# Kernel tuning notes

Measured on AMD Instinct MI355X. Metric: run time of the kernel, lower is better.

## Reference

```python
import jax, jax.numpy as jnp
import numpy as np

B, T_ENC, H2 = 32, 1024, 1024   # H2 = 2*hidden_dim
E = 128                          # embedding_dim == vocab/target size
L = 128                          # decoder timesteps (ground_truth length)
G = 4 * H2                       # LSTM gate dim
IN = E + H2                      # LSTM input dim


def setup_inputs() -> dict:
    key = jax.random.key(0)
    ks = jax.random.split(key, 6)
    s = 0.05
    return {
        "context_tensor": jax.random.normal(ks[0], (B, T_ENC, H2), jnp.float32),
        "ground_truth": jax.random.uniform(ks[1], (B, L, E), jnp.float32),
        "W_ih": jax.random.normal(ks[2], (G, IN), jnp.float32) * s,
        "W_hh": jax.random.normal(ks[3], (G, H2), jnp.float32) * s,
        "b_ih": jnp.zeros((G,), jnp.float32),
        "b_hh": jnp.zeros((G,), jnp.float32),
        "W_out": jax.random.normal(ks[4], (E, 4 * H2 // 2 * 2), jnp.float32)[:, : 2 * H2] * 0,  # placeholder overwritten below
    } | {
        "W_out": jax.random.normal(ks[4], (E, 2 * H2), jnp.float32) * s,
        "b_out": jnp.zeros((E,), jnp.float32),
    }


def reference(context_tensor, ground_truth, W_ih, W_hh, b_ih, b_hh, W_out, b_out):
    Bb, Ll, Ee = ground_truth.shape
    h2 = context_tensor.shape[-1]
    # initial <sos>: one-hot at index 0 (CreateOnehotVariable of zeros)
    onehot0 = jnp.zeros((Bb, Ee), context_tensor.dtype).at[:, 0].set(1.0)
    # input word at step i: onehot0 if i==0 else ground_truth[:, i-1]  (teacher forcing)
    words = jnp.concatenate([onehot0[:, None, :], ground_truth[:, :-1, :]], axis=1)  # [B,L,E]
    ctx0 = context_tensor[:, 0, :]  # [B,2H] -- original always concats frame 0
    xs = jnp.concatenate(
        [words, jnp.broadcast_to(ctx0[:, None, :], (Bb, Ll, h2))], axis=-1
    )  # [B,L,E+2H]
    xs = jnp.swapaxes(xs, 0, 1)  # [L,B,IN]

    def step(carry, x_t):
        h, c = carry
        gates = x_t @ W_ih.T + h @ W_hh.T + (b_ih + b_hh)  # [B,4*2H]
        i_g, f_g, g_g, o_g = jnp.split(gates, 4, axis=-1)
        c = jax.nn.sigmoid(f_g) * c + jax.nn.sigmoid(i_g) * jnp.tanh(g_g)
        h = jax.nn.sigmoid(o_g) * jnp.tanh(c)
        # dot-product attention over listener features
        energy = jnp.einsum("bh,bth->bt", h, context_tensor)
        score = jax.nn.softmax(energy, axis=-1)
        ctx = jnp.einsum("bt,bth->bh", score, context_tensor)
        feat = jnp.concatenate([h, ctx], axis=-1)  # [B,4*hidden]
        pred = jax.nn.log_softmax(feat @ W_out.T + b_out, axis=-1)  # [B,E]
        return (h, c), pred

    h0 = jnp.zeros((Bb, h2), context_tensor.dtype)
    c0 = jnp.zeros((Bb, h2), context_tensor.dtype)
    _, preds = jax.lax.scan(step, (h0, c0), xs)  # [L,B,E]
    return jnp.swapaxes(preds, 0, 1)  # [B,L,E]
```

## Files before the change

kernel.cpp:

```cpp
#include <hip/hip_runtime.h>

#define BATCH 32
#define TENC  1024
#define HD    1024
#define ED    128
#define LL    128
#define GD    4096
#define IND   1152
#define HSTEP (BATCH*HD)

#define HBUF_OFF 131072
#define ARR_OFF  (HBUF_OFF + 129*HSTEP)
#define REL_OFF  (ARR_OFF + 8192)
#define E_OFF    (REL_OFF + 64)
#define P_OFF    (E_OFF + BATCH*LL*TENC)
#define CTX_OFF  (P_OFF + BATCH*LL*TENC)
#define W16_OFF  CTX_OFF

typedef _Float16 h16x2 __attribute__((ext_vector_type(2)));
typedef __fp16   f16x2 __attribute__((ext_vector_type(2)));
typedef _Float16 f16x8v __attribute__((ext_vector_type(8)));
typedef float    f32x4v __attribute__((ext_vector_type(4)));
union CVT { f16x2 f; h16x2 h; unsigned u; };
union U4H8 { uint4 u; f16x8v h; };

__device__ __forceinline__ unsigned pk16(float x, float y) {
  CVT c; c.f = __builtin_amdgcn_cvt_pkrtz(x, y); return c.u;
}
__device__ __forceinline__ float dd2(unsigned a, unsigned b, float c) {
  CVT x{.u = a}, y{.u = b};
  return __builtin_amdgcn_fdot2(x.h, y.h, c, false);
}
__device__ __forceinline__ float sigf(float x) {
  return __builtin_amdgcn_rcpf(1.0f + __expf(-x));
}
__device__ __forceinline__ float tanhf_fast(float x) {
  return 1.0f - 2.0f * __builtin_amdgcn_rcpf(1.0f + __expf(2.0f * x));
}
__device__ __forceinline__ unsigned bfrne(float f) {
  unsigned v = __float_as_uint(f);
  return (v + 0x7fffu + ((v >> 16) & 1u)) >> 16;
}
__device__ __forceinline__ float bf2f(unsigned short u) {
  return __uint_as_float(((unsigned)u) << 16);
}
__device__ __forceinline__ void csth(unsigned short* p, unsigned short v) {
  __hip_atomic_store(p, v, __ATOMIC_RELAXED, __HIP_MEMORY_SCOPE_AGENT);
}
__device__ __forceinline__ void cstu(unsigned* p, unsigned v) {
  __hip_atomic_store(p, v, __ATOMIC_RELAXED, __HIP_MEMORY_SCOPE_AGENT);
}
__device__ __forceinline__ unsigned cldu(const unsigned* p) {
  return __hip_atomic_load(p, __ATOMIC_RELAXED, __HIP_MEMORY_SCOPE_AGENT);
}

__global__ __launch_bounds__(256) void base_kernel(
    const float* __restrict__ ctxt, const float* __restrict__ Wih,
    const float* __restrict__ bih, const float* __restrict__ bhh,
    float* __restrict__ base) {
  int id = blockIdx.x * 256 + threadIdx.x;
  int b = id & (BATCH - 1);
  int g = id >> 5;
  const float4* c4 = reinterpret_cast<const float4*>(ctxt + (size_t)b * TENC * HD);
  const float4* w4 = reinterpret_cast<const float4*>(Wih + (size_t)g * IND + ED);
  float a = 0.f;
#pragma unroll 8
  for (int kk = 0; kk < HD/4; ++kk) {
    float4 c = c4[kk], w = w4[kk];
    a += c.x*w.x + c.y*w.y + c.z*w.z + c.w*w.w;
  }
  base[(size_t)b * GD + g] = a + bih[g] + bhh[g];
}

__global__ __launch_bounds__(256) void packA_kernel(
    const float* __restrict__ Whh, float* __restrict__ ws) {
  uint4* WA = reinterpret_cast<uint4*>(ws + W16_OFF);
  const int t = blockIdx.x * 256 + threadIdx.x;
  const int l = t & 63;
  const int s = (t >> 6) & 1;
  const int w = (t >> 7) & 15;
  const int rg = t >> 11;
  const int m = l & 15;
  const int row = (m & 3) * 1024 + rg * 4 + (m >> 2);
  const int kb = 64 * w + 32 * s + (l >> 4) * 8;
  const float* src = Whh + (size_t)row * 1024 + kb;
  float4 a = *reinterpret_cast<const float4*>(src);
  float4 b = *reinterpret_cast<const float4*>(src + 4);
  uint4 o;
  o.x = pk16(a.x, a.y); o.y = pk16(a.z, a.w);
  o.z = pk16(b.x, b.y); o.w = pk16(b.z, b.w);
  WA[t] = o;
}

__global__ __launch_bounds__(256) void phase0_wordg(
    const float* __restrict__ gt, const float* __restrict__ Wih,
    float* __restrict__ ws) {
  const int mt = blockIdx.x & 31, nt = blockIdx.x >> 5;
  const int r0 = mt * 128, n0 = nt * 128;
  const int tid = threadIdx.x, tx = tid & 15, ty = tid >> 4;
  unsigned short* wg = reinterpret_cast<unsigned short*>(ws + E_OFF);
  __shared__ float At[128][18];
  __shared__ float BtT[16][132];
  float acc[8][8];
#pragma unroll
  for (int i = 0; i < 8; ++i)
#pragma unroll
    for (int j = 0; j < 8; ++j) acc[i][j] = 0.f;

  const int sr = tid >> 1, sc = (tid & 1) * 8;
  for (int kt = 0; kt < 8; ++kt) {
    const int k0 = kt * 16;
    const float* ap = Wih + (size_t)(r0 + sr) * IND + k0 + sc;
    float4 a0 = *reinterpret_cast<const float4*>(ap);
    float4 a1 = *reinterpret_cast<const float4*>(ap + 4);
    const int n = n0 + sr, t = n >> 5, bb = n & 31;
    float4 b0, b1;
    if (t == 0) {
      b0 = make_float4((k0 + sc == 0) ? 1.f : 0.f, 0.f, 0.f, 0.f);
      b1 = make_float4(0.f, 0.f, 0.f, 0.f);
    } else {
      const float* bp = gt + ((size_t)bb * LL + (t - 1)) * ED + k0 + sc;
      b0 = *reinterpret_cast<const float4*>(bp);
      b1 = *reinterpret_cast<const float4*>(bp + 4);
    }
    __syncthreads();
    *reinterpret_cast<float4*>(&At[sr][sc]) = a0;
    *reinterpret_cast<float4*>(&At[sr][sc + 4]) = a1;
    BtT[sc+0][sr] = b0.x; BtT[sc+1][sr] = b0.y; BtT[sc+2][sr] = b0.z; BtT[sc+3][sr] = b0.w;
    BtT[sc+4][sr] = b1.x; BtT[sc+5][sr] = b1.y; BtT[sc+6][sr] = b1.z; BtT[sc+7][sr] = b1.w;
    __syncthreads();
#pragma unroll
    for (int kk2 = 0; kk2 < 8; ++kk2) {
      float2 av[8];
#pragma unroll
      for (int i = 0; i < 8; ++i)
        av[i] = *reinterpret_cast<const float2*>(&At[ty*8 + i][kk2*2]);
      float4 c00 = *reinterpret_cast<const float4*>(&BtT[kk2*2][tx*8]);
      float4 c01 = *reinterpret_cast<const float4*>(&BtT[kk2*2][tx*8 + 4]);
      float4 c10 = *reinterpret_cast<const float4*>(&BtT[kk2*2+1][tx*8]);
      float4 c11 = *reinterpret_cast<const float4*>(&BtT[kk2*2+1][tx*8 + 4]);
#pragma unroll
      for (int i = 0; i < 8; ++i) {
        acc[i][0] += av[i].x*c00.x + av[i].y*c10.x;
        acc[i][1] += av[i].x*c00.y + av[i].y*c10.y;
        acc[i][2] += av[i].x*c00.z + av[i].y*c10.z;
        acc[i][3] += av[i].x*c00.w + av[i].y*c10.w;
        acc[i][4] += av[i].x*c01.x + av[i].y*c11.x;
        acc[i][5] += av[i].x*c01.y + av[i].y*c11.y;
        acc[i][6] += av[i].x*c01.z + av[i].y*c11.z;
        acc[i][7] += av[i].x*c01.w + av[i].y*c11.w;
      }
    }
  }
  const int nb = n0 + tx * 8, t = nb >> 5, b0i = nb & 31;
#pragma unroll
  for (int i = 0; i < 8; ++i) {
    const int row = r0 + ty * 8 + i;
    uint4 pk;
    pk.x = bfrne(acc[i][0]) | (bfrne(acc[i][1]) << 16);
    pk.y = bfrne(acc[i][2]) | (bfrne(acc[i][3]) << 16);
    pk.z = bfrne(acc[i][4]) | (bfrne(acc[i][5]) << 16);
    pk.w = bfrne(acc[i][6]) | (bfrne(acc[i][7]) << 16);
    *reinterpret_cast<uint4*>(wg + ((size_t)t * GD + row) * 32 + b0i) = pk;
  }
}

__global__ __launch_bounds__(1024, 4) void phaseA(float* __restrict__ ws) {
  const int rg = blockIdx.x;
  const int tid = threadIdx.x;
  const int lane = tid & 63;
  const int w = tid >> 6;
  float* base = ws;
  unsigned short* h16 = reinterpret_cast<unsigned short*>(ws + HBUF_OFF);
  unsigned* arr = reinterpret_cast<unsigned*>(ws + ARR_OFF);
  const unsigned short* wg = reinterpret_cast<const unsigned short*>(ws + E_OFF);
  const uint4* WA = reinterpret_cast<const uint4*>(ws + W16_OFF);

  extern __shared__ float smem[];
  uint4* h_lds = reinterpret_cast<uint4*>(smem);
  float* part = smem + 16384;
  float* red  = smem + 24576;

  U4H8 afr0, afr1;
  afr0.u = WA[((size_t)rg * 32 + w * 2 + 0) * 64 + lane];
  afr1.u = WA[((size_t)rg * 32 + w * 2 + 1) * 64 + lane];

  const int rT = tid >> 8, rm = (tid >> 4) & 15, rb = tid & 15;
  const int rbg = rT * 16 + rb;
  const int rrow = (rm & 3) * 1024 + rg * 4 + (rm >> 2);
  float base_r = (tid < 512) ? base[(size_t)rbg * GD + rrow] : 0.f;

  const int cjl = tid >> 5, cb = tid & 31;
  float c_reg = 0.f;

  for (int k = 0; k < LL; ++k) {
    uint4 sv[4];
    const uint4* src = reinterpret_cast<const uint4*>(h16 + (size_t)k * HSTEP);
#pragma unroll
    for (int i = 0; i < 4; ++i) sv[i] = src[tid + 1024 * i];
    float wgv = 0.f;
    if (tid < 512) wgv = bf2f(wg[((size_t)k * GD + rrow) * 32 + rbg]);
#pragma unroll
    for (int i = 0; i < 4; ++i) {
      const int u = tid + 1024 * i;
      h_lds[u ^ ((u >> 7) & 15)] = sv[i];
    }
    __syncthreads();

    f32x4v acc0 = {0.f, 0.f, 0.f, 0.f}, acc1 = acc0;
    {
      const int b0 = lane & 15, b1 = 16 + (lane & 15);
      const int k0u = 8 * w + (lane >> 4);
      U4H8 bf00, bf01, bf10, bf11;
      bf00.u = h_lds[(b0 * 128 + k0u) ^ (b0 & 15)];
      bf10.u = h_lds[(b1 * 128 + k0u) ^ (b1 & 15)];
      bf01.u = h_lds[(b0 * 128 + k0u + 4) ^ (b0 & 15)];
      bf11.u = h_lds[(b1 * 128 + k0u + 4) ^ (b1 & 15)];
      acc0 = __builtin_amdgcn_mfma_f32_16x16x32_f16(afr0.h, bf00.h, acc0, 0, 0, 0);
      acc1 = __builtin_amdgcn_mfma_f32_16x16x32_f16(afr0.h, bf10.h, acc1, 0, 0, 0);
      acc0 = __builtin_amdgcn_mfma_f32_16x16x32_f16(afr1.h, bf01.h, acc0, 0, 0, 0);
      acc1 = __builtin_amdgcn_mfma_f32_16x16x32_f16(afr1.h, bf11.h, acc1, 0, 0, 0);
    }
#pragma unroll
    for (int q = 0; q < 4; ++q) {
      const int m = (lane >> 4) * 4 + q;
      part[(m * 16 + w) * 16 + (lane & 15)] = acc0[q];
      part[((16 + m) * 16 + w) * 16 + (lane & 15)] = acc1[q];
    }
    __syncthreads();

    if (tid < 512) {
      float s = 0.f;
#pragma unroll
      for (int ww = 0; ww < 16; ++ww)
        s += part[((rT * 16 + rm) * 16 + ww) * 16 + rb];
      red[rm * 32 + rbg] = s + wgv + base_r;
    }
    __syncthreads();

    if (tid < 128) {
      float ig = sigf(red[(4 * cjl + 0) * 32 + cb]);
      float fg = sigf(red[(4 * cjl + 1) * 32 + cb]);
      float gg = tanhf_fast(red[(4 * cjl + 2) * 32 + cb]);
      float og = sigf(red[(4 * cjl + 3) * 32 + cb]);
      c_reg = fg * c_reg + ig * gg;
      float hv = og * tanhf_fast(c_reg);
      csth(h16 + (size_t)(k + 1) * HSTEP + (size_t)cb * HD + (rg * 4 + cjl),
           (unsigned short)(pk16(hv, hv) & 0xffffu));
    }

    if (k < LL - 1) {
      __syncthreads();
      const unsigned tgt = (unsigned)(k + 1);
      if (tid == 0) cstu(arr + rg * 32, tgt);
      if (tid < 64) {
        int ok;
        do {
          ok = 1;
#pragma unroll
          for (int q = 0; q < 4; ++q)
            ok &= (cldu(arr + (lane * 4 + q) * 32) >= (unsigned)tgt);
        } while (!__all(ok));
      }
      __syncthreads();
    }
  }
}

__global__ __launch_bounds__(256) void b1_energy(
    const float* __restrict__ ctxt, float* __restrict__ ws) {
  const int b = blockIdx.x >> 4, pt = blockIdx.x & 15;
  const int p0 = pt * 64;
  const int tid = threadIdx.x, tx = tid & 15, ty = tid >> 4;
  const unsigned short* h16 = reinterpret_cast<const unsigned short*>(ws + HBUF_OFF);
  float* E = ws + E_OFF;
  __shared__ unsigned At[128][8];
  __shared__ unsigned CtT[8][64];
  float acc[8][4];
#pragma unroll
  for (int i = 0; i < 8; ++i)
#pragma unroll
    for (int j = 0; j < 4; ++j) acc[i][j] = 0.f;

  const int ar = tid >> 1, ah = tid & 1;
  const int cr = tid >> 2, cq = tid & 3;
  for (int kt = 0; kt < 64; ++kt) {
    const int k0 = kt * 16;
    uint4 u = *reinterpret_cast<const uint4*>(
        h16 + (size_t)(ar + 1) * HSTEP + (size_t)b * HD + k0 + ah * 8);
    const float* cs = ctxt + ((size_t)b * TENC + p0 + cr) * HD + k0 + cq * 4;
    float4 g = *reinterpret_cast<const float4*>(cs);
    __syncthreads();
    *reinterpret_cast<uint4*>(&At[ar][ah * 4]) = u;
    CtT[2*cq][cr]   = pk16(g.x, g.y);
    CtT[2*cq+1][cr] = pk16(g.z, g.w);
    __syncthreads();
#pragma unroll
    for (int kk2 = 0; kk2 < 4; ++kk2) {
      uint2 av[8];
#pragma unroll
      for (int i = 0; i < 8; ++i)
        av[i] = *reinterpret_cast<const uint2*>(&At[ty*8 + i][kk2*2]);
      uint4 cA = *reinterpret_cast<const uint4*>(&CtT[2*kk2][tx*4]);
      uint4 cB = *reinterpret_cast<const uint4*>(&CtT[2*kk2+1][tx*4]);
#pragma unroll
      for (int i = 0; i < 8; ++i) {
        acc[i][0] = dd2(av[i].y, cB.x, dd2(av[i].x, cA.x, acc[i][0]));
        acc[i][1] = dd2(av[i].y, cB.y, dd2(av[i].x, cA.y, acc[i][1]));
        acc[i][2] = dd2(av[i].y, cB.z, dd2(av[i].x, cA.z, acc[i][2]));
        acc[i][3] = dd2(av[i].y, cB.w, dd2(av[i].x, cA.w, acc[i][3]));
      }
    }
  }
#pragma unroll
  for (int i = 0; i < 8; ++i) {
    float* ep = E + ((size_t)b * LL + ty*8 + i) * TENC + p0 + tx*4;
    *reinterpret_cast<float4*>(ep) = make_float4(acc[i][0], acc[i][1], acc[i][2], acc[i][3]);
  }
}

__global__ __launch_bounds__(1024) void b2_softmax(float* __restrict__ ws) {
  const int b = blockIdx.x >> 3, tc = blockIdx.x & 7;
  const int w = threadIdx.x >> 6, lane = threadIdx.x & 63;
  const int t = tc * 16 + w;
  const float* E = ws + E_OFF;
  unsigned* P16 = reinterpret_cast<unsigned*>(ws + P_OFF);
  const float4* e4 = reinterpret_cast<const float4*>(E + ((size_t)b * LL + t) * TENC);
  float4 v[4];
#pragma unroll
  for (int c = 0; c < 4; ++c) v[c] = e4[c * 64 + lane];
  float m = fmaxf(fmaxf(fmaxf(v[0].x, v[0].y), fmaxf(v[0].z, v[0].w)),
                  fmaxf(fmaxf(v[1].x, v[1].y), fmaxf(v[1].z, v[1].w)));
  m = fmaxf(m, fmaxf(fmaxf(fmaxf(v[2].x, v[2].y), fmaxf(v[2].z, v[2].w)),
                     fmaxf(fmaxf(v[3].x, v[3].y), fmaxf(v[3].z, v[3].w))));
#pragma unroll
  for (int o = 32; o > 0; o >>= 1) m = fmaxf(m, __shfl_xor(m, o));
  float s = 0.f;
#pragma unroll
  for (int c = 0; c < 4; ++c) {
    v[c].x = __expf(v[c].x - m); v[c].y = __expf(v[c].y - m);
    v[c].z = __expf(v[c].z - m); v[c].w = __expf(v[c].w - m);
    s += v[c].x + v[c].y + v[c].z + v[c].w;
  }
#pragma unroll
  for (int o = 32; o > 0; o >>= 1) s += __shfl_xor(s, o);
  float inv = __builtin_amdgcn_rcpf(s);
  uint2* p2 = reinterpret_cast<uint2*>(P16 + ((size_t)b * LL + t) * 512);
#pragma unroll
  for (int c = 0; c < 4; ++c) {
    uint2 o2;
    o2.x = pk16(v[c].x * inv, v[c].y * inv);
    o2.y = pk16(v[c].z * inv, v[c].w * inv);
    p2[c * 64 + lane] = o2;
  }
}

__global__ __launch_bounds__(256) void b3_ctx(
    const float* __restrict__ ctxt, float* __restrict__ ws) {
  const int b = blockIdx.x >> 4, dt = blockIdx.x & 15;
  const int d0 = dt * 64;
  const int tid = threadIdx.x, tx = tid & 15, ty = tid >> 4;
  const unsigned* P16 = reinterpret_cast<const unsigned*>(ws + P_OFF);
  unsigned* ctx16 = reinterpret_cast<unsigned*>(ws + CTX_OFF);
  __shared__ unsigned At[128][8];
  __shared__ unsigned CdT[8][64];
  float acc[8][4];
#pragma unroll
  for (int i = 0; i < 8; ++i)
#pragma unroll
    for (int j = 0; j < 4; ++j) acc[i][j] = 0.f;

  const int ar = tid >> 1, ah = tid & 1;
  const int cq = tid >> 5, cd = (tid & 31) * 2;
  for (int kt = 0; kt < 64; ++kt) {
    const int k0 = kt * 16;
    uint4 pa = *reinterpret_cast<const uint4*>(
        P16 + ((size_t)b * LL + ar) * 512 + kt * 8 + ah * 4);
    float2 r0 = *reinterpret_cast<const float2*>(
        ctxt + ((size_t)b * TENC + k0 + 2*cq) * HD + d0 + cd);
    float2 r1 = *reinterpret_cast<const float2*>(
        ctxt + ((size_t)b * TENC + k0 + 2*cq + 1) * HD + d0 + cd);
    __syncthreads();
    *reinterpret_cast<uint4*>(&At[ar][ah * 4]) = pa;
    uint2 w2;
    w2.x = pk16(r0.x, r1.x);
    w2.y = pk16(r0.y, r1.y);
    *reinterpret_cast<uint2*>(&CdT[cq][cd]) = w2;
    __syncthreads();
#pragma unroll
    for (int kk2 = 0; kk2 < 4; ++kk2) {
      uint2 av[8];
#pragma unroll
      for (int i = 0; i < 8; ++i)
        av[i] = *reinterpret_cast<const uint2*>(&At[ty*8 + i][kk2*2]);
      uint4 cA = *reinterpret_cast<const uint4*>(&CdT[2*kk2][tx*4]);
      uint4 cB = *reinterpret_cast<const uint4*>(&CdT[2*kk2+1][tx*4]);
#pragma unroll
      for (int i = 0; i < 8; ++i) {
        acc[i][0] = dd2(av[i].y, cB.x, dd2(av[i].x, cA.x, acc[i][0]));
        acc[i][1] = dd2(av[i].y, cB.y, dd2(av[i].x, cA.y, acc[i][1]));
        acc[i][2] = dd2(av[i].y, cB.z, dd2(av[i].x, cA.z, acc[i][2]));
        acc[i][3] = dd2(av[i].y, cB.w, dd2(av[i].x, cA.w, acc[i][3]));
      }
    }
  }
#pragma unroll
  for (int i = 0; i < 8; ++i) {
    uint2 o2;
    o2.x = pk16(acc[i][0], acc[i][1]);
    o2.y = pk16(acc[i][2], acc[i][3]);
    *reinterpret_cast<uint2*>(
        ctx16 + ((size_t)b * LL + ty*8 + i) * 512 + (d0 + tx*4) / 2) = o2;
  }
}

__global__ __launch_bounds__(256) void b4_logits(
    const float* __restrict__ Wout, const float* __restrict__ bout,
    const float* __restrict__ ws, float* __restrict__ out) {
  const int b = blockIdx.x >> 3, tq = blockIdx.x & 7;
  const int t0 = tq * 16;
  const int tid = threadIdx.x, tx = tid & 31, ty = tid >> 5;
  const unsigned short* h16 = reinterpret_cast<const unsigned short*>(ws + HBUF_OFF);
  const unsigned* ctx16 = reinterpret_cast<const unsigned*>(ws + CTX_OFF);
  __shared__ unsigned At[16][8];
  __shared__ unsigned WtT[8][128];
  __shared__ float lg[16][132];
  float acc[2][4];
#pragma unroll
  for (int i = 0; i < 2; ++i)
#pragma unroll
    for (int j = 0; j < 4; ++j) acc[i][j] = 0.f;

  const int wr = tid >> 1, wh = tid & 1;
  for (int kt = 0; kt < 128; ++kt) {
    const int k0 = kt * 16;
    unsigned au = 0;
    if (tid < 128) {
      const int r = tid >> 3, k = k0 + (tid & 7) * 2;
      if (k < 1024) {
        au = *reinterpret_cast<const unsigned*>(
            h16 + (size_t)(t0 + r + 1) * HSTEP + (size_t)b * HD + k);
      } else {
        au = ctx16[((size_t)b * LL + t0 + r) * 512 + (k - 1024) / 2];
      }
    }
    const float* wsrc = Wout + (size_t)wr * (2*HD) + k0 + wh * 8;
    float4 w0 = *reinterpret_cast<const float4*>(wsrc);
    float4 w1 = *reinterpret_cast<const float4*>(wsrc + 4);
    __syncthreads();
    if (tid < 128) At[tid >> 3][tid & 7] = au;
    WtT[wh*4+0][wr] = pk16(w0.x, w0.y);
    WtT[wh*4+1][wr] = pk16(w0.z, w0.w);
    WtT[wh*4+2][wr] = pk16(w1.x, w1.y);
    WtT[wh*4+3][wr] = pk16(w1.z, w1.w);
    __syncthreads();
#pragma unroll
    for (int kk2 = 0; kk2 < 4; ++kk2) {
      uint2 av[2];
#pragma unroll
      for (int i = 0; i < 2; ++i)
        av[i] = *reinterpret_cast<const uint2*>(&At[ty*2 + i][kk2*2]);
      uint4 cA = *reinterpret_cast<const uint4*>(&WtT[2*kk2][tx*4]);
      uint4 cB = *reinterpret_cast<const uint4*>(&WtT[2*kk2+1][tx*4]);
#pragma unroll
      for (int i = 0; i < 2; ++i) {
        acc[i][0] = dd2(av[i].y, cB.x, dd2(av[i].x, cA.x, acc[i][0]));
        acc[i][1] = dd2(av[i].y, cB.y, dd2(av[i].x, cA.y, acc[i][1]));
        acc[i][2] = dd2(av[i].y, cB.z, dd2(av[i].x, cA.z, acc[i][2]));
        acc[i][3] = dd2(av[i].y, cB.w, dd2(av[i].x, cA.w, acc[i][3]));
      }
    }
  }
#pragma unroll
  for (int i = 0; i < 2; ++i)
#pragma unroll
    for (int j = 0; j < 4; ++j)
      lg[ty*2 + i][tx*4 + j] = acc[i][j] + bout[tx*4 + j];
  __syncthreads();
  const int w = tid >> 6, lane = tid & 63;
#pragma unroll
  for (int rr = 0; rr < 4; ++rr) {
    const int row = w * 4 + rr;
    float v0 = lg[row][lane], v1 = lg[row][lane + 64];
    float mx = fmaxf(v0, v1);
#pragma unroll
    for (int o = 32; o > 0; o >>= 1) mx = fmaxf(mx, __shfl_xor(mx, o));
    float sm = __expf(v0 - mx) + __expf(v1 - mx);
#pragma unroll
    for (int o = 32; o > 0; o >>= 1) sm += __shfl_xor(sm, o);
    float lse = mx + __logf(sm);
    float* op = out + ((size_t)b * LL + t0 + row) * ED;
    op[lane]      = v0 - lse;
    op[lane + 64] = v1 - lse;
  }
}

extern "C" void kernel_launch(void* const* d_in, const int* in_sizes, int n_in,
                              void* d_out, int out_size, void* d_ws, size_t ws_size,
                              hipStream_t stream) {
  (void)in_sizes; (void)n_in; (void)out_size; (void)ws_size;
  const float* ctxt = (const float*)d_in[0];
  const float* gt   = (const float*)d_in[1];
  const float* Wih  = (const float*)d_in[2];
  const float* Whh  = (const float*)d_in[3];
  const float* bih  = (const float*)d_in[4];
  const float* bhh  = (const float*)d_in[5];
  const float* Wout = (const float*)d_in[6];
  const float* bout = (const float*)d_in[7];
  float* out = (float*)d_out;
  float* ws  = (float*)d_ws;

  hipMemsetAsync(ws + HBUF_OFF, 0, (size_t)HSTEP * 2, stream);
  hipMemsetAsync(ws + ARR_OFF, 0, (8192 + 64) * sizeof(float), stream);

  base_kernel<<<(BATCH * GD) / 256, 256, 0, stream>>>(ctxt, Wih, bih, bhh, ws);
  phase0_wordg<<<1024, 256, 0, stream>>>(gt, Wih, ws);
  packA_kernel<<<2048, 256, 0, stream>>>(Whh, ws);

  static int smem_set = 0;
  if (!smem_set) {
    (void)hipFuncSetAttribute((const void*)&phaseA,
                              hipFuncAttributeMaxDynamicSharedMemorySize, 100352);
    smem_set = 1;
  }
  void* argsA[] = { (void*)&ws };
  (void)hipLaunchCooperativeKernel((const void*)&phaseA, dim3(256), dim3(1024),
                                   argsA, 100352, stream);

  b1_energy<<<512, 256, 0, stream>>>(ctxt, ws);
  b2_softmax<<<256, 1024, 0, stream>>>(ws);
  b3_ctx<<<512, 256, 0, stream>>>(ctxt, ws);
  b4_logits<<<256, 256, 0, stream>>>(Wout, bout, ws, out);
}
```

Measured before the change: 989.8 us.

## Use MFMA for attention energy and context GEMMs with pre-swizzled fragment layouts

Replaces the LDS-tiled fdot2 GEMMs in the energy and context kernels with direct-from-global MFMA 16x16x32 f16 instructions. The recurrent kernel now also writes each h value into an MFMA-fragment-ordered buffer, and the softmax kernel writes probabilities in that same fragment layout, so the A operands load as single uint4 per lane. The recurrent step also folds the separate partial-sum reduction pass and its barrier into the 128 gate threads, which drops one __syncthreads per timestep. The cost is uncoalesced scattered 2-byte stores in the recurrence, strided context loads in b3, and half as many blocks for the GEMM kernels.

```diff
diff --git a/kernel.cpp b/kernel.cpp
--- a/kernel.cpp
+++ b/kernel.cpp
@@ -16,6 +16,7 @@
 #define P_OFF    (E_OFF + BATCH*LL*TENC)
 #define CTX_OFF  (P_OFF + BATCH*LL*TENC)
 #define W16_OFF  CTX_OFF
+#define HA_OFF   (CTX_OFF + 2097152)
 
 typedef _Float16 h16x2 __attribute__((ext_vector_type(2)));
 typedef __fp16   f16x2 __attribute__((ext_vector_type(2)));
@@ -175,22 +176,24 @@
   unsigned* arr = reinterpret_cast<unsigned*>(ws + ARR_OFF);
   const unsigned short* wg = reinterpret_cast<const unsigned short*>(ws + E_OFF);
   const uint4* WA = reinterpret_cast<const uint4*>(ws + W16_OFF);
+  unsigned short* HAu = reinterpret_cast<unsigned short*>(ws + HA_OFF);
 
   extern __shared__ float smem[];
   uint4* h_lds = reinterpret_cast<uint4*>(smem);
   float* part = smem + 16384;
-  float* red  = smem + 24576;
 
   U4H8 afr0, afr1;
   afr0.u = WA[((size_t)rg * 32 + w * 2 + 0) * 64 + lane];
   afr1.u = WA[((size_t)rg * 32 + w * 2 + 1) * 64 + lane];
 
-  const int rT = tid >> 8, rm = (tid >> 4) & 15, rb = tid & 15;
-  const int rbg = rT * 16 + rb;
-  const int rrow = (rm & 3) * 1024 + rg * 4 + (rm >> 2);
-  float base_r = (tid < 512) ? base[(size_t)rbg * GD + rrow] : 0.f;
-
   const int cjl = tid >> 5, cb = tid & 31;
+  const int cj = rg * 4 + cjl;
+  float bs4[4];
+  if (tid < 128) {
+#pragma unroll
+    for (int g = 0; g < 4; ++g)
+      bs4[g] = base[(size_t)cb * GD + g * HD + cj];
+  }
   float c_reg = 0.f;
 
   for (int k = 0; k < LL; ++k) {
@@ -198,8 +201,6 @@
     const uint4* src = reinterpret_cast<const uint4*>(h16 + (size_t)k * HSTEP);
 #pragma unroll
     for (int i = 0; i < 4; ++i) sv[i] = src[tid + 1024 * i];
-    float wgv = 0.f;
-    if (tid < 512) wgv = bf2f(wg[((size_t)k * GD + rrow) * 32 + rbg]);
 #pragma unroll
     for (int i = 0; i < 4; ++i) {
       const int u = tid + 1024 * i;
@@ -225,28 +226,33 @@
     for (int q = 0; q < 4; ++q) {
       const int m = (lane >> 4) * 4 + q;
       part[(m * 16 + w) * 16 + (lane & 15)] = acc0[q];
-      part[((16 + m) * 16 + w) * 16 + (lane & 15)] = acc1[q];
+      part[4096 + (m * 16 + w) * 16 + (lane & 15)] = acc1[q];
     }
     __syncthreads();
 
-    if (tid < 512) {
-      float s = 0.f;
-#pragma unroll
-      for (int ww = 0; ww < 16; ++ww)
-        s += part[((rT * 16 + rm) * 16 + ww) * 16 + rb];
-      red[rm * 32 + rbg] = s + wgv + base_r;
-    }
-    __syncthreads();
-
     if (tid < 128) {
-      float ig = sigf(red[(4 * cjl + 0) * 32 + cb]);
-      float fg = sigf(red[(4 * cjl + 1) * 32 + cb]);
-      float gg = tanhf_fast(red[(4 * cjl + 2) * 32 + cb]);
-      float og = sigf(red[(4 * cjl + 3) * 32 + cb]);
+      const int T = cb >> 4, b16 = cb & 15;
+      float s[4];
+#pragma unroll
+      for (int g = 0; g < 4; ++g) {
+        const int m = 4 * cjl + g;
+        float acc = 0.f;
+#pragma unroll
+        for (int ww = 0; ww < 16; ++ww)
+          acc += part[T * 4096 + (m * 16 + ww) * 16 + b16];
+        s[g] = acc + bf2f(wg[((size_t)k * GD + g * HD + cj) * 32 + cb]) + bs4[g];
+      }
+      float ig = sigf(s[0]);
+      float fg = sigf(s[1]);
+      float gg = tanhf_fast(s[2]);
+      float og = sigf(s[3]);
       c_reg = fg * c_reg + ig * gg;
       float hv = og * tanhf_fast(c_reg);
-      csth(h16 + (size_t)(k + 1) * HSTEP + (size_t)cb * HD + (rg * 4 + cjl),
-           (unsigned short)(pk16(hv, hv) & 0xffffu));
+      unsigned short hu = (unsigned short)(pk16(hv, hv) & 0xffffu);
+      csth(h16 + (size_t)(k + 1) * HSTEP + (size_t)cb * HD + cj, hu);
+      const size_t unit = (((size_t)cb * 8 + (k >> 4)) * 32 + (cj >> 5)) * 64
+                          + ((cj >> 3) & 3) * 16 + (k & 15);
+      HAu[unit * 8 + (cj & 7)] = hu;
     }
 
     if (k < LL - 1) {
@@ -269,54 +275,44 @@
 
 __global__ __launch_bounds__(256) void b1_energy(
     const float* __restrict__ ctxt, float* __restrict__ ws) {
-  const int b = blockIdx.x >> 4, pt = blockIdx.x & 15;
-  const int p0 = pt * 64;
-  const int tid = threadIdx.x, tx = tid & 15, ty = tid >> 4;
-  const unsigned short* h16 = reinterpret_cast<const unsigned short*>(ws + HBUF_OFF);
+  const int b = blockIdx.x >> 3, pt = blockIdx.x & 7;
+  const int lane = threadIdx.x & 63, w = threadIdx.x >> 6;
+  const int p0 = pt * 128 + w * 32;
+  const uint4* HA = reinterpret_cast<const uint4*>(ws + HA_OFF);
   float* E = ws + E_OFF;
-  __shared__ unsigned At[128][8];
-  __shared__ unsigned CtT[8][64];
-  float acc[8][4];
-#pragma unroll
-  for (int i = 0; i < 8; ++i)
-#pragma unroll
-    for (int j = 0; j < 4; ++j) acc[i][j] = 0.f;
-
-  const int ar = tid >> 1, ah = tid & 1;
-  const int cr = tid >> 2, cq = tid & 3;
-  for (int kt = 0; kt < 64; ++kt) {
-    const int k0 = kt * 16;
-    uint4 u = *reinterpret_cast<const uint4*>(
-        h16 + (size_t)(ar + 1) * HSTEP + (size_t)b * HD + k0 + ah * 8);
-    const float* cs = ctxt + ((size_t)b * TENC + p0 + cr) * HD + k0 + cq * 4;
-    float4 g = *reinterpret_cast<const float4*>(cs);
-    __syncthreads();
-    *reinterpret_cast<uint4*>(&At[ar][ah * 4]) = u;
-    CtT[2*cq][cr]   = pk16(g.x, g.y);
-    CtT[2*cq+1][cr] = pk16(g.z, g.w);
-    __syncthreads();
-#pragma unroll
-    for (int kk2 = 0; kk2 < 4; ++kk2) {
-      uint2 av[8];
-#pragma unroll
-      for (int i = 0; i < 8; ++i)
-        av[i] = *reinterpret_cast<const uint2*>(&At[ty*8 + i][kk2*2]);
-      uint4 cA = *reinterpret_cast<const uint4*>(&CtT[2*kk2][tx*4]);
-      uint4 cB = *reinterpret_cast<const uint4*>(&CtT[2*kk2+1][tx*4]);
-#pragma unroll
-      for (int i = 0; i < 8; ++i) {
-        acc[i][0] = dd2(av[i].y, cB.x, dd2(av[i].x, cA.x, acc[i][0]));
-        acc[i][1] = dd2(av[i].y, cB.y, dd2(av[i].x, cA.y, acc[i][1]));
-        acc[i][2] = dd2(av[i].y, cB.z, dd2(av[i].x, cA.z, acc[i][2]));
-        acc[i][3] = dd2(av[i].y, cB.w, dd2(av[i].x, cA.w, acc[i][3]));
-      }
-    }
-  }
-#pragma unroll
-  for (int i = 0; i < 8; ++i) {
-    float* ep = E + ((size_t)b * LL + ty*8 + i) * TENC + p0 + tx*4;
-    *reinterpret_cast<float4*>(ep) = make_float4(acc[i][0], acc[i][1], acc[i][2], acc[i][3]);
-  }
+  f32x4v acc[8][2];
+#pragma unroll
+  for (int i = 0; i < 8; ++i) { acc[i][0] = {0,0,0,0}; acc[i][1] = {0,0,0,0}; }
+
+  const float* c0 = ctxt + ((size_t)b * TENC + p0 + (lane & 15)) * HD + (lane >> 4) * 8;
+  const float* c1 = c0 + 16 * HD;
+  const uint4* hab = HA + (size_t)b * 8 * 32 * 64 + lane;
+  for (int ks = 0; ks < 32; ++ks) {
+    float4 x0 = *reinterpret_cast<const float4*>(c0 + ks * 32);
+    float4 x1 = *reinterpret_cast<const float4*>(c0 + ks * 32 + 4);
+    float4 y0 = *reinterpret_cast<const float4*>(c1 + ks * 32);
+    float4 y1 = *reinterpret_cast<const float4*>(c1 + ks * 32 + 4);
+    U4H8 bf0, bf1;
+    bf0.u.x = pk16(x0.x, x0.y); bf0.u.y = pk16(x0.z, x0.w);
+    bf0.u.z = pk16(x1.x, x1.y); bf0.u.w = pk16(x1.z, x1.w);
+    bf1.u.x = pk16(y0.x, y0.y); bf1.u.y = pk16(y0.z, y0.w);
+    bf1.u.z = pk16(y1.x, y1.y); bf1.u.w = pk16(y1.z, y1.w);
+    const uint4* ha = hab + (size_t)ks * 64;
+#pragma unroll
+    for (int mt = 0; mt < 8; ++mt) {
+      U4H8 af; af.u = ha[(size_t)mt * 2048];
+      acc[mt][0] = __builtin_amdgcn_mfma_f32_16x16x32_f16(af.h, bf0.h, acc[mt][0], 0, 0, 0);
+      acc[mt][1] = __builtin_amdgcn_mfma_f32_16x16x32_f16(af.h, bf1.h, acc[mt][1], 0, 0, 0);
+    }
+  }
+#pragma unroll
+  for (int mt = 0; mt < 8; ++mt)
+#pragma unroll
+    for (int q = 0; q < 4; ++q) {
+      const int t = mt * 16 + (lane >> 4) * 4 + q;
+      E[((size_t)b * LL + t) * TENC + p0 + (lane & 15)] = acc[mt][0][q];
+      E[((size_t)b * LL + t) * TENC + p0 + 16 + (lane & 15)] = acc[mt][1][q];
+    }
 }
 
 __global__ __launch_bounds__(1024) void b2_softmax(float* __restrict__ ws) {
@@ -324,7 +320,7 @@
   const int w = threadIdx.x >> 6, lane = threadIdx.x & 63;
   const int t = tc * 16 + w;
   const float* E = ws + E_OFF;
-  unsigned* P16 = reinterpret_cast<unsigned*>(ws + P_OFF);
+  unsigned* PA32 = reinterpret_cast<unsigned*>(ws + P_OFF);
   const float4* e4 = reinterpret_cast<const float4*>(E + ((size_t)b * LL + t) * TENC);
   float4 v[4];
 #pragma unroll
@@ -345,73 +341,61 @@
 #pragma unroll
   for (int o = 32; o > 0; o >>= 1) s += __shfl_xor(s, o);
   float inv = __builtin_amdgcn_rcpf(s);
-  uint2* p2 = reinterpret_cast<uint2*>(P16 + ((size_t)b * LL + t) * 512);
 #pragma unroll
   for (int c = 0; c < 4; ++c) {
+    const int p = (c * 64 + lane) * 4;
     uint2 o2;
     o2.x = pk16(v[c].x * inv, v[c].y * inv);
     o2.y = pk16(v[c].z * inv, v[c].w * inv);
-    p2[c * 64 + lane] = o2;
+    const size_t unit = (((size_t)b * 8 + tc) * 32 + (p >> 5)) * 64
+                        + ((p >> 3) & 3) * 16 + w;
+    *reinterpret_cast<uint2*>(PA32 + unit * 4 + ((p & 7) >> 1)) = o2;
   }
 }
 
 __global__ __launch_bounds__(256) void b3_ctx(
     const float* __restrict__ ctxt, float* __restrict__ ws) {
-  const int b = blockIdx.x >> 4, dt = blockIdx.x & 15;
-  const int d0 = dt * 64;
-  const int tid = threadIdx.x, tx = tid & 15, ty = tid >> 4;
-  const unsigned* P16 = reinterpret_cast<const unsigned*>(ws + P_OFF);
-  unsigned* ctx16 = reinterpret_cast<unsigned*>(ws + CTX_OFF);
-  __shared__ unsigned At[128][8];
-  __shared__ unsigned CdT[8][64];
-  float acc[8][4];
-#pragma unroll
-  for (int i = 0; i < 8; ++i)
-#pragma unroll
-    for (int j = 0; j < 4; ++j) acc[i][j] = 0.f;
-
-  const int ar = tid >> 1, ah = tid & 1;
-  const int cq = tid >> 5, cd = (tid & 31) * 2;
-  for (int kt = 0; kt < 64; ++kt) {
-    const int k0 = kt * 16;
-    uint4 pa = *reinterpret_cast<const uint4*>(
-        P16 + ((size_t)b * LL + ar) * 512 + kt * 8 + ah * 4);
-    float2 r0 = *reinterpret_cast<const float2*>(
-        ctxt + ((size_t)b * TENC + k0 + 2*cq) * HD + d0 + cd);
-    float2 r1 = *reinterpret_cast<const float2*>(
-        ctxt + ((size_t)b * TENC + k0 + 2*cq + 1) * HD + d0 + cd);
-    __syncthreads();
-    *reinterpret_cast<uint4*>(&At[ar][ah * 4]) = pa;
-    uint2 w2;
-    w2.x = pk16(r0.x, r1.x);
-    w2.y = pk16(r0.y, r1.y);
-    *reinterpret_cast<uint2*>(&CdT[cq][cd]) = w2;
-    __syncthreads();
-#pragma unroll
-    for (int kk2 = 0; kk2 < 4; ++kk2) {
-      uint2 av[8];
-#pragma unroll
-      for (int i = 0; i < 8; ++i)
-        av[i] = *reinterpret_cast<const uint2*>(&At[ty*8 + i][kk2*2]);
-      uint4 cA = *reinterpret_cast<const uint4*>(&CdT[2*kk2][tx*4]);
-      uint4 cB = *reinterpret_cast<const uint4*>(&CdT[2*kk2+1][tx*4]);
-#pragma unroll
-      for (int i = 0; i < 8; ++i) {
-        acc[i][0] = dd2(av[i].y, cB.x, dd2(av[i].x, cA.x, acc[i][0]));
-        acc[i][1] = dd2(av[i].y, cB.y, dd2(av[i].x, cA.y, acc[i][1]));
-        acc[i][2] = dd2(av[i].y, cB.z, dd2(av[i].x, cA.z, acc[i][2]));
-        acc[i][3] = dd2(av[i].y, cB.w, dd2(av[i].x, cA.w, acc[i][3]));
-      }
-    }
-  }
-#pragma unroll
-  for (int i = 0; i < 8; ++i) {
-    uint2 o2;
-    o2.x = pk16(acc[i][0], acc[i][1]);
-    o2.y = pk16(acc[i][2], acc[i][3]);
-    *reinterpret_cast<uint2*>(
-        ctx16 + ((size_t)b * LL + ty*8 + i) * 512 + (d0 + tx*4) / 2) = o2;
-  }
+  const int b = blockIdx.x >> 3, dt = blockIdx.x & 7;
+  const int lane = threadIdx.x & 63, w = threadIdx.x >> 6;
+  const int d0 = dt * 128 + w * 32;
+  const uint4* PA = reinterpret_cast<const uint4*>(ws + P_OFF);
+  unsigned short* ctx16u = reinterpret_cast<unsigned short*>(ws + CTX_OFF);
+  f32x4v acc[8][2];
+#pragma unroll
+  for (int i = 0; i < 8; ++i) { acc[i][0] = {0,0,0,0}; acc[i][1] = {0,0,0,0}; }
+
+  const float* cb0 = ctxt + (size_t)b * TENC * HD + d0 + (lane & 15);
+  const uint4* pab = PA + (size_t)b * 8 * 32 * 64 + lane;
+  for (int ks = 0; ks < 32; ++ks) {
+    const int pbase = ks * 32 + (lane >> 4) * 8;
+    U4H8 bf0, bf1;
+#pragma unroll
+    for (int jj = 0; jj < 4; ++jj) {
+      const float* r0 = cb0 + (size_t)(pbase + 2 * jj) * HD;
+      const float* r1 = r0 + HD;
+      unsigned u0 = pk16(r0[0], r1[0]);
+      unsigned u1 = pk16(r0[16], r1[16]);
+      (&bf0.u.x)[jj] = u0;
+      (&bf1.u.x)[jj] = u1;
+    }
+    const uint4* pa = pab + (size_t)ks * 64;
+#pragma unroll
+    for (int mt = 0; mt < 8; ++mt) {
+      U4H8 af; af.u = pa[(size_t)mt * 2048];
+      acc[mt][0] = __builtin_amdgcn_mfma_f32_16x16x32_f16(af.h, bf0.h, acc[mt][0], 0, 0, 0);
+      acc[mt][1] = __builtin_amdgcn_mfma_f32_16x16x32_f16(af.h, bf1.h, acc[mt][1], 0, 0, 0);
+    }
+  }
+#pragma unroll
+  for (int mt = 0; mt < 8; ++mt)
+#pragma unroll
+    for (int q = 0; q < 4; ++q) {
+      const int t = mt * 16 + (lane >> 4) * 4 + q;
+      ctx16u[((size_t)b * LL + t) * 1024 + d0 + (lane & 15)] =
+          (unsigned short)(pk16(acc[mt][0][q], acc[mt][0][q]) & 0xffffu);
+      ctx16u[((size_t)b * LL + t) * 1024 + d0 + 16 + (lane & 15)] =
+          (unsigned short)(pk16(acc[mt][1][q], acc[mt][1][q]) & 0xffffu);
+    }
 }
 
 __global__ __launch_bounds__(256) void b4_logits(
@@ -520,15 +504,15 @@
   static int smem_set = 0;
   if (!smem_set) {
     (void)hipFuncSetAttribute((const void*)&phaseA,
-                              hipFuncAttributeMaxDynamicSharedMemorySize, 100352);
+                              hipFuncAttributeMaxDynamicSharedMemorySize, 98304);
     smem_set = 1;
   }
   void* argsA[] = { (void*)&ws };
   (void)hipLaunchCooperativeKernel((const void*)&phaseA, dim3(256), dim3(1024),
-                                   argsA, 100352, stream);
-
-  b1_energy<<<512, 256, 0, stream>>>(ctxt, ws);
+                                   argsA, 98304, stream);
+
+  b1_energy<<<256, 256, 0, stream>>>(ctxt, ws);
   b2_softmax<<<256, 1024, 0, stream>>>(ws);
-  b3_ctx<<<512, 256, 0, stream>>>(ctxt, ws);
+  b3_ctx<<<256, 256, 0, stream>>>(ctxt, ws);
   b4_logits<<<256, 256, 0, stream>>>(Wout, bout, ws, out);
 }
```

Measured after the change: 875.8 us. -11.5%, faster.
